# Kernel tuning notes

Hardware: AMD Instinct MI355X
Metric: run time of the kernel (lower is better)

The kernel has to match this reference:

```python
import jax, jax.numpy as jnp
import numpy as np

N = 16384   # total nodes
G = 256     # graphs in batch
E0 = 131072 # random edges (self loops appended, matching PyG add_self_loops=True)
IN = 256
H = 8       # heads
F = 64      # per-head out dim (h1=h2=h3)


def setup_inputs() -> dict:
    key = jax.random.key(0)
    ks = jax.random.split(key, 40)
    nrm = lambda k, shape, s=0.05: jax.random.normal(k, shape, jnp.float32) * s
    x = jax.random.normal(ks[0], (N, IN), jnp.float32)
    src0 = jax.random.randint(ks[1], (E0,), 0, N)
    dst0 = jax.random.randint(ks[2], (E0,), 0, N)
    loop = jnp.arange(N)
    inp = dict(
        x=x,
        edge_src=jnp.concatenate([src0, loop]),
        edge_dst=jnp.concatenate([dst0, loop]),
        batch=jnp.repeat(jnp.arange(G), N // G),
    )
    dims_in = [IN, H * F, H * F]
    norm_dim = [H * F, H * F, F]
    bias_dim = [H * F, H * F, F]  # conv3 concat=False -> bias size F
    ki = 3
    for i in range(3):
        d = dims_in[i]
        inp[f'Wl{i+1}'] = nrm(ks[ki], (d, H * F)); ki += 1
        inp[f'Wr{i+1}'] = nrm(ks[ki], (d, H * F)); ki += 1
        inp[f'att{i+1}'] = nrm(ks[ki], (H, F)); ki += 1
        inp[f'b{i+1}'] = nrm(ks[ki], (bias_dim[i],)); ki += 1
        inp[f'gnw{i+1}'] = jnp.ones((norm_dim[i],), jnp.float32)
        inp[f'gnb{i+1}'] = jnp.zeros((norm_dim[i],), jnp.float32)
        inp[f'gnm{i+1}'] = jnp.ones((norm_dim[i],), jnp.float32)
    inp['Wlin'] = nrm(ks[ki], (F, 2)); ki += 1
    inp['blin'] = jnp.zeros((2,), jnp.float32)
    return inp


def _gatv2(x, Wl, Wr, att, b, src, dst, concat):
    # GATv2Conv (PyG defaults: share_weights=False, negative_slope=0.2), eval mode (no dropout)
    n = x.shape[0]
    Hh, Ff = att.shape
    xl = (x @ Wl).reshape(n, Hh, Ff)
    xr = (x @ Wr).reshape(n, Hh, Ff)
    m = xl[src] + xr[dst]                      # [E, H, F]
    e = jnp.where(m > 0, m, 0.2 * m)           # leaky_relu
    logit = jnp.einsum('ehf,hf->eh', e, att)   # [E, H]
    lmax = jax.ops.segment_max(logit, dst, num_segments=n)
    lmax = jnp.where(jnp.isneginf(lmax), 0.0, lmax)
    p = jnp.exp(logit - lmax[dst])
    den = jax.ops.segment_sum(p, dst, num_segments=n)
    alpha = p / (den[dst] + 1e-16)             # PyG softmax eps
    out = jax.ops.segment_sum(alpha[:, :, None] * xl[src], dst, num_segments=n)
    out = out.reshape(n, Hh * Ff) if concat else out.mean(axis=1)
    return out + b


def _graphnorm(x, w, b, ms, batch, g):
    cnt = jax.ops.segment_sum(jnp.ones((x.shape[0],), x.dtype), batch, num_segments=g)[:, None]
    mean = jax.ops.segment_sum(x, batch, num_segments=g) / cnt
    xc = x - ms * mean[batch]
    var = jax.ops.segment_sum(xc * xc, batch, num_segments=g) / cnt
    return w * xc / jnp.sqrt(var[batch] + 1e-5) + b


def reference(x, edge_src, edge_dst, batch,
              Wl1, Wr1, att1, b1, gnw1, gnb1, gnm1,
              Wl2, Wr2, att2, b2, gnw2, gnb2, gnm2,
              Wl3, Wr3, att3, b3, gnw3, gnb3, gnm3,
              Wlin, blin):
    h = jax.nn.relu(_graphnorm(_gatv2(x, Wl1, Wr1, att1, b1, edge_src, edge_dst, True), gnw1, gnb1, gnm1, batch, G))
    h = jax.nn.relu(_graphnorm(_gatv2(h, Wl2, Wr2, att2, b2, edge_src, edge_dst, True), gnw2, gnb2, gnm2, batch, G))
    h = jax.nn.relu(_graphnorm(_gatv2(h, Wl3, Wr3, att3, b3, edge_src, edge_dst, False), gnw3, gnb3, gnm3, batch, G))
    cnt = jax.ops.segment_sum(jnp.ones((h.shape[0],), h.dtype), batch, num_segments=G)[:, None]
    pooled = jax.ops.segment_sum(h, batch, num_segments=G) / cnt  # global_mean_pool
    return pooled @ Wlin + blin
```

## Files before the change

### kernel.cpp

```cpp
#include <hip/hip_runtime.h>
#include <hip/hip_bf16.h>
#include <stdint.h>
#include <string.h>

#define NNODES 16384
#define GIN 256
#define NG 64
#define NGRAPH 256
#define FDIM 64
#define CDIM 512

typedef __attribute__((ext_vector_type(8))) short bf16x8;
typedef __attribute__((ext_vector_type(4))) float f32x4;

__device__ __forceinline__ float bf2f(unsigned short u){
  union { unsigned int i; float f; } w; w.i = ((unsigned int)u) << 16; return w.f;
}

__device__ __forceinline__ void unpk(unsigned int u, float& lo, float& hi){
  union { unsigned int i; float f; } a, b;
  a.i = u << 16; b.i = u & 0xffff0000u;
  lo = a.f; hi = b.f;
}

union PK8 { __hip_bfloat16 h[8]; uint4 v; };

__device__ __forceinline__ void async16(const void* g, void* l){
  __builtin_amdgcn_global_load_lds(
      (const __attribute__((address_space(1))) unsigned int*)g,
      (__attribute__((address_space(3))) unsigned int*)l, 16, 0, 0);
}

__global__ void k_detect(const unsigned short* __restrict__ x, int* __restrict__ flag){
  int lane = threadIdx.x;
  int bad = 0;
  #pragma unroll
  for (int j = 0; j < 4; j++){
    float f = bf2f(x[lane*4 + j]);
    if (!(fabsf(f) < 1e4f)) bad++;
  }
  #pragma unroll
  for (int o = 32; o; o >>= 1) bad += __shfl_down(bad, o);
  if (lane == 0) *flag = (bad > 16) ? 1 : 0;
}

struct CArgs {
  const void* p[17];
  int cum[18];
};

__global__ void k_convert(CArgs a, const int* __restrict__ flag, float* __restrict__ dst, int total){
  int isf32 = *flag;
  for (int idx = blockIdx.x*blockDim.x + threadIdx.x; idx < total; idx += gridDim.x*blockDim.x){
    int seg = 0;
    while (idx >= a.cum[seg+1]) seg++;
    int off = idx - a.cum[seg];
    float v;
    if (isf32) v = ((const float*)a.p[seg])[off];
    else       v = bf2f(((const unsigned short*)a.p[seg])[off]);
    dst[idx] = v;
  }
}

__global__ void k_xconv(const void* __restrict__ xin, const int* __restrict__ flag,
                        __hip_bfloat16* __restrict__ xbf, int* __restrict__ deg, int total){
  int isf32 = *flag;
  for (int idx = blockIdx.x*blockDim.x + threadIdx.x; idx < total; idx += gridDim.x*blockDim.x){
    if (idx < NNODES) deg[idx] = 0;
    float v;
    if (isf32) v = ((const float*)xin)[idx];
    else       v = bf2f(((const unsigned short*)xin)[idx]);
    xbf[idx] = __float2bfloat16(v);
  }
}

struct TArgs {
  const void* W[6];
  __hip_bfloat16* Wt[6];
  int K[6];
};

__global__ void k_transpose_all(TArgs t, const int* __restrict__ flag){
  int isf32 = *flag;
  int seg = blockIdx.z;
  int K = t.K[seg];
  int n0 = blockIdx.x*32, k0 = blockIdx.y*32;
  if (k0 >= K) return;
  const void* W = t.W[seg];
  __hip_bfloat16* Wt = t.Wt[seg];
  __shared__ float tl[32][33];
  for (int r = threadIdx.y; r < 32; r += 8){
    size_t idx = (size_t)(k0 + r)*CDIM + n0 + threadIdx.x;
    tl[r][threadIdx.x] = isf32 ? ((const float*)W)[idx] : bf2f(((const unsigned short*)W)[idx]);
  }
  __syncthreads();
  for (int r = threadIdx.y; r < 32; r += 8)
    Wt[(size_t)(n0 + r)*K + k0 + threadIdx.x] = __float2bfloat16(tl[threadIdx.x][r]);
}

__global__ void k_count(const int* __restrict__ edst, int E, int* __restrict__ deg){
  int e = blockIdx.x*blockDim.x + threadIdx.x;
  if (e < E) atomicAdd(&deg[edst[e]], 1);
}

__global__ void k_scan(const int* __restrict__ deg, int* __restrict__ off, int* __restrict__ cur){
  __shared__ int ss[256];
  int t = threadIdx.x;
  int base = t * 64;
  int s = 0;
  for (int j = 0; j < 64; j++) s += deg[base + j];
  ss[t] = s;
  __syncthreads();
  for (int o = 1; o < 256; o <<= 1){
    int v = 0;
    if (t >= o) v = ss[t - o];
    __syncthreads();
    if (t >= o) ss[t] += v;
    __syncthreads();
  }
  int run = ss[t] - s;
  for (int j = 0; j < 64; j++){
    int i = base + j;
    off[i] = run;
    cur[i] = run;
    run += deg[i];
  }
  if (t == 255) off[NNODES] = run;
}

__global__ void k_fill(const int* __restrict__ esrc, const int* __restrict__ edst, int E,
                       int* __restrict__ cur, int* __restrict__ srcs){
  int e = blockIdx.x*blockDim.x + threadIdx.x;
  if (e < E){
    int pos = atomicAdd(&cur[edst[e]], 1);
    srcs[pos] = esrc[e];
  }
}

__global__ __launch_bounds__(256) void k_gemm_mfma(
    const __hip_bfloat16* __restrict__ A,
    const __hip_bfloat16* __restrict__ Wtl, const __hip_bfloat16* __restrict__ Wtr,
    __hip_bfloat16* __restrict__ Cl, __hip_bfloat16* __restrict__ Cr, int K){
  const __hip_bfloat16* Wt = blockIdx.z ? Wtr : Wtl;
  __hip_bfloat16*       C  = blockIdx.z ? Cr  : Cl;
  __shared__ __align__(16) char As[2][16384];
  __shared__ __align__(16) char Bs[2][16384];
  int tid = threadIdx.x;
  int w = tid >> 6, lane = tid & 63;
  int wm = (w >> 1) & 1, wn = w & 1;
  int row0 = blockIdx.x * 128, col0 = blockIdx.y * 128;
  int c = lane >> 4, l16 = lane & 15;

  f32x4 acc[4][4];
  #pragma unroll
  for (int i = 0; i < 4; i++)
    #pragma unroll
    for (int j = 0; j < 4; j++) acc[i][j] = (f32x4){0.f,0.f,0.f,0.f};

  auto stage = [&](int buf, int k0){
    #pragma unroll
    for (int t = 0; t < 8; t++){
      int call = t*4 + w;
      if (call < 16){
        int cc = call >> 1, half = call & 1;
        const __hip_bfloat16* gp = A + (size_t)(row0 + half*64 + lane)*K + k0 + cc*8;
        async16(gp, As[buf] + call*1024);
      } else {
        int q = call - 16;
        int cc = q >> 1, half = q & 1;
        const __hip_bfloat16* gp = Wt + (size_t)(col0 + half*64 + lane)*K + k0 + cc*8;
        async16(gp, Bs[buf] + q*1024);
      }
    }
  };

  stage(0, 0);
  __syncthreads();

  int nIter = K >> 6;
  for (int it = 0; it < nIter; it++){
    int cur = it & 1;
    bf16x8 af[2][4], bfr[2][4];
    #pragma unroll
    for (int ko = 0; ko < 2; ko++){
      #pragma unroll
      for (int i = 0; i < 4; i++)
        af[ko][i]  = *(const bf16x8*)(As[cur] + (ko*4 + c)*2048 + (wm*64 + i*16 + l16)*16);
      #pragma unroll
      for (int j = 0; j < 4; j++)
        bfr[ko][j] = *(const bf16x8*)(Bs[cur] + (ko*4 + c)*2048 + (wn*64 + j*16 + l16)*16);
    }
    if (it + 1 < nIter) stage(1 - cur, (it + 1) << 6);
    #pragma unroll
    for (int ko = 0; ko < 2; ko++)
      #pragma unroll
      for (int i = 0; i < 4; i++)
        #pragma unroll
        for (int j = 0; j < 4; j++)
          acc[i][j] = __builtin_amdgcn_mfma_f32_16x16x32_bf16(af[ko][i], bfr[ko][j], acc[i][j], 0, 0, 0);
    __syncthreads();
  }

  int r4 = lane >> 4;
  #pragma unroll
  for (int i = 0; i < 4; i++)
    #pragma unroll
    for (int j = 0; j < 4; j++){
      __hip_bfloat16* cp = C + (size_t)(row0 + wm*64 + i*16 + r4*4)*CDIM + col0 + wn*64 + j*16 + l16;
      #pragma unroll
      for (int r = 0; r < 4; r++)
        cp[(size_t)r*CDIM] = __float2bfloat16(acc[i][j][r]);
    }
}

template<int CONCAT>
__global__ __launch_bounds__(256) void k_fused_attn(
    const __hip_bfloat16* __restrict__ XL, const __hip_bfloat16* __restrict__ XR,
    const float* __restrict__ att,
    const int* __restrict__ off, const int* __restrict__ srcs,
    const float* __restrict__ bias, __hip_bfloat16* __restrict__ OUT){
  int wave = threadIdx.x >> 6, lane = threadIdx.x & 63;
  int d = blockIdx.x * 4 + wave;
  if (d >= NNODES) return;

  uint4 xru = *(const uint4*)((const char*)XR + ((size_t)d*CDIM + lane*8)*2);
  float xr[8];
  unpk(xru.x, xr[0], xr[1]); unpk(xru.y, xr[2], xr[3]);
  unpk(xru.z, xr[4], xr[5]); unpk(xru.w, xr[6], xr[7]);
  const float4* atp = (const float4*)(att + lane*8);
  float4 at0 = atp[0], at1 = atp[1];
  float at[8] = {at0.x, at0.y, at0.z, at0.w, at1.x, at1.y, at1.z, at1.w};

  float acc[8];
  #pragma unroll
  for (int j = 0; j < 8; j++) acc[j] = 0.f;
  float den = 0.f;

  int beg = off[d], end = off[d+1];

  auto leaky = [](float m){ return fmaxf(m, 0.2f*m); };

  for (int i = beg; i < end; i += 4){
    int n = end - i;
    int s0 = srcs[i];
    int s1 = n > 1 ? srcs[i+1] : s0;
    int s2 = n > 2 ? srcs[i+2] : s0;
    int s3 = n > 3 ? srcs[i+3] : s0;
    uint4 rw[4];
    rw[0] = *(const uint4*)((const char*)XL + ((size_t)s0*CDIM + lane*8)*2);
    rw[1] = *(const uint4*)((const char*)XL + ((size_t)s1*CDIM + lane*8)*2);
    rw[2] = *(const uint4*)((const char*)XL + ((size_t)s2*CDIM + lane*8)*2);
    rw[3] = *(const uint4*)((const char*)XL + ((size_t)s3*CDIM + lane*8)*2);

    #pragma unroll
    for (int e = 0; e < 4; e++){
      if (e < n){
        float xv[8];
        unpk(rw[e].x, xv[0], xv[1]);
        unpk(rw[e].y, xv[2], xv[3]);
        unpk(rw[e].z, xv[4], xv[5]);
        unpk(rw[e].w, xv[6], xv[7]);
        float v = 0.f;
        #pragma unroll
        for (int j = 0; j < 8; j++) v = fmaf(leaky(xv[j] + xr[j]), at[j], v);
        v += __shfl_xor(v, 1); v += __shfl_xor(v, 2); v += __shfl_xor(v, 4);
        float p = expf(v);
        den += p;
        #pragma unroll
        for (int j = 0; j < 8; j++) acc[j] = fmaf(p, xv[j], acc[j]);
      }
    }
  }

  float inv = 1.f / (den + 1e-16f);
  const float4* bp = (const float4*)(bias + (CONCAT ? lane*8 : (lane & 7)*8));

  if (CONCAT){
    float4 b0v = bp[0], b1v = bp[1];
    float bb[8] = {b0v.x, b0v.y, b0v.z, b0v.w, b1v.x, b1v.y, b1v.z, b1v.w};
    PK8 pk;
    #pragma unroll
    for (int j = 0; j < 8; j++)
      pk.h[j] = __float2bfloat16(acc[j]*inv + bb[j]);
    *(uint4*)((char*)OUT + ((size_t)d*CDIM + lane*8)*2) = pk.v;
  } else {
    float r[8];
    #pragma unroll
    for (int j = 0; j < 8; j++) r[j] = acc[j] * inv;
    #pragma unroll
    for (int o = 8; o < 64; o <<= 1)
      #pragma unroll
      for (int j = 0; j < 8; j++) r[j] += __shfl_xor(r[j], o);
    if (lane < 8){
      float4 b0v = bp[0], b1v = bp[1];
      float bb[8] = {b0v.x, b0v.y, b0v.z, b0v.w, b1v.x, b1v.y, b1v.z, b1v.w};
      PK8 pk;
      #pragma unroll
      for (int j = 0; j < 8; j++)
        pk.h[j] = __float2bfloat16(r[j]*0.125f + bb[j]);
      *(uint4*)((char*)OUT + ((size_t)d*FDIM + lane*8)*2) = pk.v;
    }
  }
}

__global__ void k_graphnorm_relu(const __hip_bfloat16* __restrict__ X, const float* __restrict__ w,
    const float* __restrict__ b, const float* __restrict__ ms,
    __hip_bfloat16* __restrict__ Y, int C){
  int g = blockIdx.x;
  int c = threadIdx.x;
  const __hip_bfloat16* xg = X + (size_t)g * NG * C + c;
  __hip_bfloat16* yg = Y + (size_t)g * NG * C + c;
  float v[NG];
  float s1 = 0.f, s2 = 0.f;
  #pragma unroll
  for (int i = 0; i < NG; i++){
    v[i] = __bfloat162float(xg[(size_t)i*C]);
    s1 += v[i]; s2 += v[i]*v[i];
  }
  float mean = s1 * (1.f/NG);
  float m = ms[c];
  float var = s2 * (1.f/NG) - 2.f*m*mean*mean + m*m*mean*mean;
  float inv = rsqrtf(var + 1e-5f);
  float ww = w[c], bb = b[c];
  #pragma unroll
  for (int i = 0; i < NG; i++){
    float y = fmaf(ww * (v[i] - m*mean), inv, bb);
    yg[(size_t)i*C] = __float2bfloat16(y > 0.f ? y : 0.f);
  }
}

__global__ void k_pool_linear(const __hip_bfloat16* __restrict__ H, const float* __restrict__ Wlin,
    const float* __restrict__ blin, void* out, const int* __restrict__ flag){
  int g = blockIdx.x, c = threadIdx.x;
  float s = 0.f;
  for (int i = 0; i < NG; i++) s += __bfloat162float(H[(long)(g*NG + i)*FDIM + c]);
  float pooled = s * (1.f/NG);
  float v0 = pooled * Wlin[c*2 + 0];
  float v1 = pooled * Wlin[c*2 + 1];
  #pragma unroll
  for (int o = 32; o; o >>= 1){ v0 += __shfl_down(v0, o); v1 += __shfl_down(v1, o); }
  if (c == 0){
    float o0 = v0 + blin[0], o1 = v1 + blin[1];
    if (*flag){
      ((float*)out)[g*2 + 0] = o0;
      ((float*)out)[g*2 + 1] = o1;
    } else {
      ((__hip_bfloat16*)out)[g*2 + 0] = __float2bfloat16(o0);
      ((__hip_bfloat16*)out)[g*2 + 1] = __float2bfloat16(o1);
    }
  }
}

extern "C" void kernel_launch(void* const* d_in, const int* in_sizes, int n_in,
                              void* d_out, int out_size, void* d_ws, size_t ws_size,
                              hipStream_t stream){
  const int N = NNODES;
  const int E = in_sizes[1];

  const int* esrc = (const int*)d_in[1];
  const int* edst = (const int*)d_in[2];

  char* ws = (char*)d_ws;
  size_t cursor_b = 0;
  auto alloc = [&](size_t bytes)->char*{
    char* p = ws + cursor_b;
    cursor_b += (bytes + 255) & ~size_t(255);
    return p;
  };

  int* flag = (int*)alloc(256);

  static const int convIdx[17] = {6,7,8,9,10, 13,14,15,16,17, 20,21,22,23,24, 25,26};
  CArgs ca;
  int cums[18]; cums[0] = 0;
  for (int i = 0; i < 17; i++){
    ca.p[i] = d_in[convIdx[i]];
    cums[i+1] = cums[i] + in_sizes[convIdx[i]];
  }
  memcpy(ca.cum, cums, sizeof(cums));
  int totalConv = cums[17];

  float* conv = (float*)alloc((size_t)totalConv * 4);
  const float* fw[17];
  for (int i = 0; i < 17; i++) fw[i] = conv + cums[i];

  __hip_bfloat16* XLbf  = (__hip_bfloat16*)alloc((size_t)N * CDIM * 2);
  __hip_bfloat16* XRbf  = (__hip_bfloat16*)alloc((size_t)N * CDIM * 2);
  __hip_bfloat16* OUTbf = (__hip_bfloat16*)alloc((size_t)N * CDIM * 2);
  __hip_bfloat16* OUT3  = (__hip_bfloat16*)alloc((size_t)N * FDIM * 2);
  __hip_bfloat16* HBbf  = (__hip_bfloat16*)alloc((size_t)N * CDIM * 2);
  __hip_bfloat16* xbf   = (__hip_bfloat16*)alloc((size_t)N * GIN * 2);
  __hip_bfloat16* Wt[6];
  Wt[0] = (__hip_bfloat16*)alloc((size_t)CDIM * GIN * 2);
  Wt[1] = (__hip_bfloat16*)alloc((size_t)CDIM * GIN * 2);
  Wt[2] = (__hip_bfloat16*)alloc((size_t)CDIM * CDIM * 2);
  Wt[3] = (__hip_bfloat16*)alloc((size_t)CDIM * CDIM * 2);
  Wt[4] = (__hip_bfloat16*)alloc((size_t)CDIM * CDIM * 2);
  Wt[5] = (__hip_bfloat16*)alloc((size_t)CDIM * CDIM * 2);
  int* deg  = (int*)alloc((size_t)N * 4);
  int* off  = (int*)alloc((size_t)(N + 1) * 4);
  int* cur  = (int*)alloc((size_t)N * 4);
  int* srcs = (int*)alloc((size_t)E * 4);

  k_detect<<<1, 64, 0, stream>>>((const unsigned short*)d_in[0], flag);
  k_convert<<<32, 256, 0, stream>>>(ca, flag, conv, totalConv);
  k_xconv<<<2048, 256, 0, stream>>>(d_in[0], flag, xbf, deg, N * GIN);
  {
    TArgs ta;
    const void* Ws[6] = {d_in[4], d_in[5], d_in[11], d_in[12], d_in[18], d_in[19]};
    const int   Ks[6] = {GIN, GIN, CDIM, CDIM, CDIM, CDIM};
    for (int i = 0; i < 6; i++){ ta.W[i] = Ws[i]; ta.Wt[i] = Wt[i]; ta.K[i] = Ks[i]; }
    k_transpose_all<<<dim3(CDIM/32, CDIM/32, 6), dim3(32, 8), 0, stream>>>(ta, flag);
  }

  k_count<<<(E + 255)/256, 256, 0, stream>>>(edst, E, deg);
  k_scan<<<1, 256, 0, stream>>>(deg, off, cur);
  k_fill<<<(E + 255)/256, 256, 0, stream>>>(esrc, edst, E, cur, srcs);

  const float* att_[3] = {fw[0],  fw[5],  fw[10]};
  const float* b_[3]   = {fw[1],  fw[6],  fw[11]};
  const float* gw_[3]  = {fw[2],  fw[7],  fw[12]};
  const float* gb_[3]  = {fw[3],  fw[8],  fw[13]};
  const float* gm_[3]  = {fw[4],  fw[9],  fw[14]};

  const __hip_bfloat16* inbuf = xbf;
  int K = GIN;
  for (int layer = 0; layer < 3; layer++){
    k_gemm_mfma<<<dim3(N/128, CDIM/128, 2), 256, 0, stream>>>(
        inbuf, Wt[layer*2], Wt[layer*2 + 1], XLbf, XRbf, K);
    if (layer < 2){
      k_fused_attn<1><<<N/4, 256, 0, stream>>>(XLbf, XRbf, att_[layer], off, srcs, b_[layer], OUTbf);
      k_graphnorm_relu<<<NGRAPH, CDIM, 0, stream>>>(OUTbf, gw_[layer], gb_[layer], gm_[layer], HBbf, CDIM);
    } else {
      k_fused_attn<0><<<N/4, 256, 0, stream>>>(XLbf, XRbf, att_[layer], off, srcs, b_[layer], OUT3);
      k_graphnorm_relu<<<NGRAPH, FDIM, 0, stream>>>(OUT3, gw_[layer], gb_[layer], gm_[layer], HBbf, FDIM);
    }
    inbuf = HBbf;
    K = CDIM;
  }

  k_pool_linear<<<NGRAPH, 64, 0, stream>>>(HBbf, fw[15], fw[16], d_out, flag);
}
```

Measured before the change: 363.8 us.

## Single-buffer GEMM LDS tiles and widen attention edge gather to eight

The MFMA GEMM drops double-buffered shared memory and now loads each K tile synchronously before computing. This halves LDS use, which may allow more blocks per CU, but gives up overlap of global loads with MFMA work. Separately, the attention kernel gathers eight source rows per iteration instead of four, so more memory loads are in flight per wave at the cost of more registers.

```diff
diff --git a/kernel.cpp b/kernel.cpp
--- a/kernel.cpp
+++ b/kernel.cpp
@@ -143,11 +143,11 @@
     __hip_bfloat16* __restrict__ Cl, __hip_bfloat16* __restrict__ Cr, int K){
   const __hip_bfloat16* Wt = blockIdx.z ? Wtr : Wtl;
   __hip_bfloat16*       C  = blockIdx.z ? Cr  : Cl;
-  __shared__ __align__(16) char As[2][16384];
-  __shared__ __align__(16) char Bs[2][16384];
+  __shared__ __align__(16) char As[16384];
+  __shared__ __align__(16) char Bs[16384];
   int tid = threadIdx.x;
   int w = tid >> 6, lane = tid & 63;
-  int wm = (w >> 1) & 1, wn = w & 1;
+  int wm = w >> 1, wn = w & 1;
   int row0 = blockIdx.x * 128, col0 = blockIdx.y * 128;
   int c = lane >> 4, l16 = lane & 15;
 
@@ -157,47 +157,37 @@
     #pragma unroll
     for (int j = 0; j < 4; j++) acc[i][j] = (f32x4){0.f,0.f,0.f,0.f};
 
-  auto stage = [&](int buf, int k0){
+  for (int k0 = 0; k0 < K; k0 += 64){
     #pragma unroll
     for (int t = 0; t < 8; t++){
       int call = t*4 + w;
       if (call < 16){
         int cc = call >> 1, half = call & 1;
         const __hip_bfloat16* gp = A + (size_t)(row0 + half*64 + lane)*K + k0 + cc*8;
-        async16(gp, As[buf] + call*1024);
+        async16(gp, As + call*1024);
       } else {
         int q = call - 16;
         int cc = q >> 1, half = q & 1;
         const __hip_bfloat16* gp = Wt + (size_t)(col0 + half*64 + lane)*K + k0 + cc*8;
-        async16(gp, Bs[buf] + q*1024);
+        async16(gp, Bs + q*1024);
       }
     }
-  };
-
-  stage(0, 0);
-  __syncthreads();
-
-  int nIter = K >> 6;
-  for (int it = 0; it < nIter; it++){
-    int cur = it & 1;
-    bf16x8 af[2][4], bfr[2][4];
+    __syncthreads();
     #pragma unroll
     for (int ko = 0; ko < 2; ko++){
+      bf16x8 af[4], bfr[4];
       #pragma unroll
       for (int i = 0; i < 4; i++)
-        af[ko][i]  = *(const bf16x8*)(As[cur] + (ko*4 + c)*2048 + (wm*64 + i*16 + l16)*16);
+        af[i]  = *(const bf16x8*)(As + (ko*4 + c)*2048 + (wm*64 + i*16 + l16)*16);
       #pragma unroll
       for (int j = 0; j < 4; j++)
-        bfr[ko][j] = *(const bf16x8*)(Bs[cur] + (ko*4 + c)*2048 + (wn*64 + j*16 + l16)*16);
-    }
-    if (it + 1 < nIter) stage(1 - cur, (it + 1) << 6);
-    #pragma unroll
-    for (int ko = 0; ko < 2; ko++)
+        bfr[j] = *(const bf16x8*)(Bs + (ko*4 + c)*2048 + (wn*64 + j*16 + l16)*16);
       #pragma unroll
       for (int i = 0; i < 4; i++)
         #pragma unroll
         for (int j = 0; j < 4; j++)
-          acc[i][j] = __builtin_amdgcn_mfma_f32_16x16x32_bf16(af[ko][i], bfr[ko][j], acc[i][j], 0, 0, 0);
+          acc[i][j] = __builtin_amdgcn_mfma_f32_16x16x32_bf16(af[i], bfr[j], acc[i][j], 0, 0, 0);
+    }
     __syncthreads();
   }
 
@@ -240,20 +230,18 @@
 
   auto leaky = [](float m){ return fmaxf(m, 0.2f*m); };
 
-  for (int i = beg; i < end; i += 4){
+  for (int i = beg; i < end; i += 8){
     int n = end - i;
-    int s0 = srcs[i];
-    int s1 = n > 1 ? srcs[i+1] : s0;
-    int s2 = n > 2 ? srcs[i+2] : s0;
-    int s3 = n > 3 ? srcs[i+3] : s0;
-    uint4 rw[4];
-    rw[0] = *(const uint4*)((const char*)XL + ((size_t)s0*CDIM + lane*8)*2);
-    rw[1] = *(const uint4*)((const char*)XL + ((size_t)s1*CDIM + lane*8)*2);
-    rw[2] = *(const uint4*)((const char*)XL + ((size_t)s2*CDIM + lane*8)*2);
-    rw[3] = *(const uint4*)((const char*)XL + ((size_t)s3*CDIM + lane*8)*2);
-
-    #pragma unroll
-    for (int e = 0; e < 4; e++){
+    int sidx[8];
+    #pragma unroll
+    for (int e = 0; e < 8; e++) sidx[e] = (e < n) ? srcs[i + e] : sidx[0];
+    uint4 rw[8];
+    #pragma unroll
+    for (int e = 0; e < 8; e++)
+      rw[e] = *(const uint4*)((const char*)XL + ((size_t)sidx[e]*CDIM + lane*8)*2);
+
+    #pragma unroll
+    for (int e = 0; e < 8; e++){
       if (e < n){
         float xv[8];
         unpk(rw[e].x, xv[0], xv[1]);
```

Result: no change. 365.0 us (+0.3%).
